# Kernel optimization log

Hardware: AMD Instinct MI355X
Metric: run time of the kernel (lower is better)

## Reference

```python
import jax, jax.numpy as jnp
import numpy as np

NLVL = 8
C = 64          # channel_siz
FIN = 16        # in_filter_siz  = in_siz  / 2**nlvl
FOUT = 16       # out_filter_siz = out_siz / 2**nlvl
B = 512
IN_SIZ = 4096
STD = 0.1  # keeps 8 relu-matmul levels numerically stable (0.1*sqrt(2C)~1.1 gain/level)


def setup_inputs() -> dict:
    key = jax.random.key(0)
    k0, k1, k2, k3, k4, k5 = jax.random.split(key, 6)
    n_lvl_filters = 2 ** (NLVL + 1) - 2  # 510: level lvl occupies [2^lvl-2 : 2^(lvl+1)-2]
    return {
        "in_data": jax.random.normal(k0, (B, IN_SIZ), dtype=jnp.float32),
        "W_in": jax.random.normal(k1, (FIN, C), dtype=jnp.float32) * STD,
        "b_in": jax.random.normal(k2, (C,), dtype=jnp.float32) * STD,
        "W_lvl": jax.random.normal(k3, (n_lvl_filters, 2, C, C), dtype=jnp.float32) * STD,
        "b_lvl": jax.random.normal(k4, (n_lvl_filters, C), dtype=jnp.float32) * STD,
        "Fea": jax.random.normal(k5, (2 ** NLVL, C, FOUT), dtype=jnp.float32) * STD,
    }


def reference(in_data, W_in, b_in, W_lvl, b_lvl, Fea):
    b = in_data.shape[0]
    # Input interpolation: conv1d(filter (FIN,1,C), stride FIN) on (b, 2^nlvl*FIN, 1)
    # == per-block matmul on (b, 2^nlvl, FIN).
    x = in_data.reshape(b, 2 ** NLVL, FIN)
    V = jax.nn.relu(jnp.einsum("bkf,fc->bkc", x, W_in) + b_in)  # (b, 2^nlvl, C)
    # State V: (b, K, T, C) where K = 2^lvl boxes, T = 2^(nlvl-lvl) positions.
    V = V[:, None]  # lvl 0: (b, 1, 2^nlvl, C)
    for lvl in range(1, NLVL + 1):
        K = 2 ** lvl
        off = K - 2
        W = W_lvl[off:off + K]          # (K, 2, C, C)
        bb = b_lvl[off:off + K]         # (K, C)
        T = V.shape[2] // 2
        pairs = V.reshape(b, K // 2, T, 2, C)      # stride-2 conv pairs
        pairs = jnp.repeat(pairs, 2, axis=1)       # both children share the parent
        V = jax.nn.relu(jnp.einsum("bktsc,kscd->bktd", pairs, W) + bb[:, None, :])
    # Output dense per box: (b, 2^nlvl, C) x (2^nlvl, C, FOUT)
    out = jnp.einsum("bkc,kcf->bkf", V[:, :, 0, :], Fea)
    return out.reshape(b, 2 ** NLVL * FOUT, 1)
```

## Files before the change

### kernel.cpp

```cpp
#include <hip/hip_runtime.h>

typedef __attribute__((ext_vector_type(8))) short short8;
typedef __attribute__((ext_vector_type(4))) float f32x4;

#define NLVL 8
#define C64 64

__device__ __forceinline__ unsigned short f2bf(float f) {
    union { float f; unsigned u; } v; v.f = f;
    unsigned r = v.u + 0x7FFFu + ((v.u >> 16) & 1u);
    return (unsigned short)(r >> 16);
}
__device__ __forceinline__ float bf2f(unsigned short h) {
    union { unsigned u; float f; } v; v.u = ((unsigned)h) << 16;
    return v.f;
}

__global__ __launch_bounds__(256) void k_convw(const float* __restrict__ W_lvl,
                                               unsigned short* __restrict__ Wt) {
    __shared__ float buf[128 * 65];
    const int kf = blockIdx.x;
    const int i  = threadIdx.x;
    const float* src = W_lvl + (size_t)kf * 8192;
    for (int m = 0; m < 32; ++m) {
        int idx = m * 256 + i;
        int kin = idx >> 6, d = idx & 63;
        buf[kin * 65 + d] = src[idx];
    }
    __syncthreads();
    unsigned short* dst = Wt + (size_t)kf * 16384;
    for (int m = 0; m < 64; ++m) {
        int o = m * 256 + i;
        int d = o >> 8;
        int kin2 = o & 255;
        int kin = kin2 & 127;
        float val = buf[kin * 65 + d];
        unsigned short hi = f2bf(val);
        unsigned short outv = (kin2 >> 7) ? f2bf(val - bf2f(hi)) : hi;
        dst[o] = outv;
    }
}

__global__ __launch_bounds__(256) void k_lvl0(const float* __restrict__ x,
                                              const float* __restrict__ W_in,
                                              const float* __restrict__ b_in,
                                              unsigned short* __restrict__ V0) {
    __shared__ float wl[16 * 64];
    __shared__ float bl[64];
    __shared__ float xl[16 * 16];
    const int i = threadIdx.x;
    for (int m = 0; m < 4; ++m) wl[m * 256 + i] = W_in[m * 256 + i];
    if (i < 64) bl[i] = b_in[i];
    const int row0 = blockIdx.x * 16;
    xl[i] = x[(size_t)row0 * 16 + i];
    __syncthreads();
    const int r  = i >> 4;
    const int c0 = (i & 15) * 4;
    float a0 = bl[c0], a1 = bl[c0 + 1], a2 = bl[c0 + 2], a3 = bl[c0 + 3];
#pragma unroll
    for (int f = 0; f < 16; ++f) {
        float xv = xl[r * 16 + f];
        const float* wrow = &wl[f * 64 + c0];
        a0 += xv * wrow[0]; a1 += xv * wrow[1]; a2 += xv * wrow[2]; a3 += xv * wrow[3];
    }
    size_t ob = (size_t)(row0 + r) * 64 + c0;
    V0[ob]     = f2bf(fmaxf(a0, 0.f));
    V0[ob + 1] = f2bf(fmaxf(a1, 0.f));
    V0[ob + 2] = f2bf(fmaxf(a2, 0.f));
    V0[ob + 3] = f2bf(fmaxf(a3, 0.f));
}

__global__ __launch_bounds__(256) void k_level(const unsigned short* __restrict__ Vprev,
                                               unsigned short* __restrict__ Vnext,
                                               const unsigned short* __restrict__ Wt,
                                               const float* __restrict__ b_lvl,
                                               int lvl) {
    extern __shared__ unsigned short wlds[];
    const int T   = 1 << (8 - lvl);
    const int lgT = 8 - lvl;
    const int off = (1 << lvl) - 2;
    const int parent = blockIdx.y;
    const int tid = threadIdx.x;

    {
        const uint4* gsrc = (const uint4*)(Wt + (size_t)(off + 2 * parent) * 16384);
        uint4* ldst = (uint4*)wlds;
#pragma unroll
        for (int m = 0; m < 16; ++m) {
            int p = m * 256 + tid;
            uint4 v = gsrc[p];
            int sw = p ^ ((p >> 5) & 7);
            ldst[sw] = v;
        }
    }
    __syncthreads();

    const int w  = tid >> 6;
    const int l  = tid & 63;
    const int q  = l >> 4;
    const int ln = l & 15;

    const int r_global = blockIdx.x * 64 + w * 16 + ln;
    const int b  = r_global >> lgT;
    const int t  = r_global & (T - 1);
    const unsigned short* Abase =
        Vprev + ((size_t)b << 14) + (size_t)parent * ((size_t)T << 7) + (size_t)t * 128 + q * 8;

    short8 a[4];
#pragma unroll
    for (int kk = 0; kk < 4; ++kk)
        a[kk] = *(const short8*)(Abase + kk * 32);

    f32x4 acc[2][4];
    f32x4 zero = {0.f, 0.f, 0.f, 0.f};
#pragma unroll
    for (int s = 0; s < 2; ++s)
#pragma unroll
        for (int nt = 0; nt < 4; ++nt) acc[s][nt] = zero;

#pragma unroll
    for (int s = 0; s < 2; ++s) {
#pragma unroll
        for (int nt = 0; nt < 4; ++nt) {
            const int d = nt * 16 + ln;
#pragma unroll
            for (int kk = 0; kk < 8; ++kk) {
                int ch = (s << 11) + (d << 5) + (kk << 2) + q;
                ch ^= (d & 7);
                short8 bfrag = *(const short8*)((const unsigned short*)wlds + ch * 8);
                acc[s][nt] = __builtin_amdgcn_mfma_f32_16x16x32_bf16(
                    a[kk & 3], bfrag, acc[s][nt], 0, 0, 0);
            }
        }
    }

#pragma unroll
    for (int s = 0; s < 2; ++s) {
        const int kf_local = 2 * parent + s;
        const float* brow = b_lvl + (size_t)(off + kf_local) * 64;
#pragma unroll
        for (int nt = 0; nt < 4; ++nt) {
            float bias = brow[nt * 16 + ln];
#pragma unroll
            for (int j = 0; j < 4; ++j) {
                int rl = w * 16 + q * 4 + j;
                int rg = blockIdx.x * 64 + rl;
                int bb = rg >> lgT;
                int tt = rg & (T - 1);
                float v = fmaxf(acc[s][nt][j] + bias, 0.f);
                Vnext[((size_t)bb << 14) + (size_t)kf_local * ((size_t)T << 6) +
                      (size_t)tt * 64 + nt * 16 + ln] = f2bf(v);
            }
        }
    }
}

__global__ __launch_bounds__(256) void k_final(const unsigned short* __restrict__ V8,
                                               const float* __restrict__ Fea,
                                               float* __restrict__ out) {
    __shared__ float fl[64 * 16];
    __shared__ unsigned short vl[16 * 64];
    const int k  = blockIdx.x;
    const int b0 = blockIdx.y * 16;
    const int i  = threadIdx.x;
    for (int m = 0; m < 4; ++m) fl[m * 256 + i] = Fea[(size_t)k * 1024 + m * 256 + i];
    {
        int idx = i * 4;
        int bl2 = idx >> 6, c = idx & 63;
        const unsigned short* src = V8 + ((size_t)(b0 + bl2) << 14) + k * 64 + c;
        *(uint2*)&vl[idx] = *(const uint2*)src;
    }
    __syncthreads();
    const int bl2 = i >> 4, f = i & 15;
    float acc = 0.f;
#pragma unroll
    for (int c = 0; c < 64; ++c)
        acc += bf2f(vl[bl2 * 64 + c]) * fl[c * 16 + f];
    out[(size_t)(b0 + bl2) * 4096 + (size_t)k * 16 + f] = acc;
}

extern "C" void kernel_launch(void* const* d_in, const int* in_sizes, int n_in,
                              void* d_out, int out_size, void* d_ws, size_t ws_size,
                              hipStream_t stream) {
    const float* in_data = (const float*)d_in[0];
    const float* W_in    = (const float*)d_in[1];
    const float* b_in    = (const float*)d_in[2];
    const float* W_lvl   = (const float*)d_in[3];
    const float* b_lvl   = (const float*)d_in[4];
    const float* Fea     = (const float*)d_in[5];
    float* out = (float*)d_out;

    unsigned short* Wt = (unsigned short*)d_ws;
    unsigned short* Va = (unsigned short*)((char*)d_ws + 16711680);
    unsigned short* Vb = (unsigned short*)((char*)d_ws + 16711680 + 16777216);

    k_convw<<<510, 256, 0, stream>>>(W_lvl, Wt);
    k_lvl0<<<8192, 256, 0, stream>>>(in_data, W_in, b_in, Va);

    const unsigned short* cur = Va;
    unsigned short* nxt = Vb;
    for (int lvl = 1; lvl <= NLVL; ++lvl) {
        int T = 1 << (8 - lvl);
        dim3 grid(8 * T, 1 << (lvl - 1));
        k_level<<<grid, 256, 65536, stream>>>(cur, nxt, Wt, b_lvl, lvl);
        unsigned short* tmp = (unsigned short*)cur;
        cur = nxt;
        nxt = tmp;
    }
    k_final<<<dim3(256, 32), 256, 0, stream>>>(cur, Fea, out);
}
```

Measured before the change: 219.8 us.

## Hold level weights in registers per wave instead of staging through LDS

The level kernel stops copying the 64KB weight tile for each parent into shared memory. Each wave now owns a 16-column output slice and loads its B fragments for both children straight into registers. It then loops over four 16-row M tiles, reusing those fragments. This removes the LDS fill, the barrier and the 64KB dynamic LDS allocation that capped occupancy, and adds a launch bound of 3 blocks. In exchange each wave reads its A rows four times from global/L2 and needs many more VGPRs for the register-held weights.

```diff
diff --git a/kernel.cpp b/kernel.cpp
--- a/kernel.cpp
+++ b/kernel.cpp
@@ -4,7 +4,6 @@
 typedef __attribute__((ext_vector_type(4))) float f32x4;
 
 #define NLVL 8
-#define C64 64
 
 __device__ __forceinline__ unsigned short f2bf(float f) {
     union { float f; unsigned u; } v; v.f = f;
@@ -70,87 +69,64 @@
     V0[ob + 3] = f2bf(fmaxf(a3, 0.f));
 }
 
-__global__ __launch_bounds__(256) void k_level(const unsigned short* __restrict__ Vprev,
-                                               unsigned short* __restrict__ Vnext,
-                                               const unsigned short* __restrict__ Wt,
-                                               const float* __restrict__ b_lvl,
-                                               int lvl) {
-    extern __shared__ unsigned short wlds[];
+__global__ __launch_bounds__(256, 3) void k_level(const unsigned short* __restrict__ Vprev,
+                                                  unsigned short* __restrict__ Vnext,
+                                                  const unsigned short* __restrict__ Wt,
+                                                  const float* __restrict__ b_lvl,
+                                                  int lvl) {
     const int T   = 1 << (8 - lvl);
     const int lgT = 8 - lvl;
     const int off = (1 << lvl) - 2;
-    const int parent = blockIdx.y;
+    const int p   = blockIdx.y;
     const int tid = threadIdx.x;
+    const int w   = tid >> 6;
+    const int l   = tid & 63;
+    const int q   = l >> 4;
+    const int ln  = l & 15;
 
+    short8 bw[2][8];
     {
-        const uint4* gsrc = (const uint4*)(Wt + (size_t)(off + 2 * parent) * 16384);
-        uint4* ldst = (uint4*)wlds;
+        const unsigned short* wbase =
+            Wt + (size_t)(off + 2 * p) * 16384 + (size_t)(w * 16 + ln) * 256 + q * 8;
 #pragma unroll
-        for (int m = 0; m < 16; ++m) {
-            int p = m * 256 + tid;
-            uint4 v = gsrc[p];
-            int sw = p ^ ((p >> 5) & 7);
-            ldst[sw] = v;
-        }
+        for (int s = 0; s < 2; ++s)
+#pragma unroll
+            for (int kk = 0; kk < 8; ++kk)
+                bw[s][kk] = *(const short8*)(wbase + s * 16384 + kk * 32);
     }
-    __syncthreads();
+    const float bias0 = b_lvl[(off + 2 * p) * 64 + w * 16 + ln];
+    const float bias1 = b_lvl[(off + 2 * p + 1) * 64 + w * 16 + ln];
 
-    const int w  = tid >> 6;
-    const int l  = tid & 63;
-    const int q  = l >> 4;
-    const int ln = l & 15;
+#pragma unroll 2
+    for (int m = 0; m < 4; ++m) {
+        const int r = blockIdx.x * 64 + m * 16 + ln;
+        const int b = r >> lgT;
+        const int t = r & (T - 1);
+        const unsigned short* Abase =
+            Vprev + ((size_t)b << 14) + ((size_t)p << (lgT + 7)) + (size_t)t * 128 + q * 8;
+        short8 a[4];
+#pragma unroll
+        for (int kk = 0; kk < 4; ++kk)
+            a[kk] = *(const short8*)(Abase + kk * 32);
 
-    const int r_global = blockIdx.x * 64 + w * 16 + ln;
-    const int b  = r_global >> lgT;
-    const int t  = r_global & (T - 1);
-    const unsigned short* Abase =
-        Vprev + ((size_t)b << 14) + (size_t)parent * ((size_t)T << 7) + (size_t)t * 128 + q * 8;
-
-    short8 a[4];
+        f32x4 acc0 = {0.f, 0.f, 0.f, 0.f};
+        f32x4 acc1 = {0.f, 0.f, 0.f, 0.f};
 #pragma unroll
-    for (int kk = 0; kk < 4; ++kk)
-        a[kk] = *(const short8*)(Abase + kk * 32);
-
-    f32x4 acc[2][4];
-    f32x4 zero = {0.f, 0.f, 0.f, 0.f};
+        for (int kk = 0; kk < 8; ++kk)
+            acc0 = __builtin_amdgcn_mfma_f32_16x16x32_bf16(a[kk & 3], bw[0][kk], acc0, 0, 0, 0);
 #pragma unroll
-    for (int s = 0; s < 2; ++s)
-#pragma unroll
-        for (int nt = 0; nt < 4; ++nt) acc[s][nt] = zero;
+        for (int kk = 0; kk < 8; ++kk)
+            acc1 = __builtin_amdgcn_mfma_f32_16x16x32_bf16(a[kk & 3], bw[1][kk], acc1, 0, 0, 0);
 
 #pragma unroll
-    for (int s = 0; s < 2; ++s) {
-#pragma unroll
-        for (int nt = 0; nt < 4; ++nt) {
-            const int d = nt * 16 + ln;
-#pragma unroll
-            for (int kk = 0; kk < 8; ++kk) {
-                int ch = (s << 11) + (d << 5) + (kk << 2) + q;
-                ch ^= (d & 7);
-                short8 bfrag = *(const short8*)((const unsigned short*)wlds + ch * 8);
-                acc[s][nt] = __builtin_amdgcn_mfma_f32_16x16x32_bf16(
-                    a[kk & 3], bfrag, acc[s][nt], 0, 0, 0);
-            }
-        }
-    }
-
-#pragma unroll
-    for (int s = 0; s < 2; ++s) {
-        const int kf_local = 2 * parent + s;
-        const float* brow = b_lvl + (size_t)(off + kf_local) * 64;
-#pragma unroll
-        for (int nt = 0; nt < 4; ++nt) {
-            float bias = brow[nt * 16 + ln];
-#pragma unroll
-            for (int j = 0; j < 4; ++j) {
-                int rl = w * 16 + q * 4 + j;
-                int rg = blockIdx.x * 64 + rl;
-                int bb = rg >> lgT;
-                int tt = rg & (T - 1);
-                float v = fmaxf(acc[s][nt][j] + bias, 0.f);
-                Vnext[((size_t)bb << 14) + (size_t)kf_local * ((size_t)T << 6) +
-                      (size_t)tt * 64 + nt * 16 + ln] = f2bf(v);
-            }
+        for (int j = 0; j < 4; ++j) {
+            const int rg = blockIdx.x * 64 + m * 16 + q * 4 + j;
+            const int bb = rg >> lgT;
+            const int tt = rg & (T - 1);
+            const size_t base = ((size_t)bb << 14) + (size_t)(2 * p) * ((size_t)T << 6) +
+                                (size_t)tt * 64 + w * 16 + ln;
+            Vnext[base] = f2bf(fmaxf(acc0[j] + bias0, 0.f));
+            Vnext[base + ((size_t)T << 6)] = f2bf(fmaxf(acc1[j] + bias1, 0.f));
         }
     }
 }
@@ -202,7 +178,7 @@
     for (int lvl = 1; lvl <= NLVL; ++lvl) {
         int T = 1 << (8 - lvl);
         dim3 grid(8 * T, 1 << (lvl - 1));
-        k_level<<<grid, 256, 65536, stream>>>(cur, nxt, Wt, b_lvl, lvl);
+        k_level<<<grid, 256, 0, stream>>>(cur, nxt, Wt, b_lvl, lvl);
         unsigned short* tmp = (unsigned short*)cur;
         cur = nxt;
         nxt = tmp;
```

Result: slower. 257.6 us (+17.2%).
